# Optimization experiments

Hardware: AMD Instinct MI355X
Metric: run time of the kernel (lower is better)

Reference implementation:

```python
import jax, jax.numpy as jnp
import numpy as np

# dims
B, NB, T, NC = 16, 55, 512, 8          # batch, filter bands, time steps, CSP comps
D, L, H, E, K, F, C = 512, 6, 8, 8, 2, 2048, 2  # embed, depth, heads, experts, top_k, d_ff, classes
DH = D // H
IN = NB * NC  # 440
EPS = 1e-5


def _ln(x, s, b):
    m = x.mean(-1, keepdims=True)
    v = ((x - m) ** 2).mean(-1, keepdims=True)
    return (x - m) / jnp.sqrt(v + EPS) * s + b


def setup_inputs() -> dict:
    key = jax.random.key(0)
    ks = iter(jax.random.split(key, 64))
    n = lambda shape, s=0.02: jax.random.normal(next(ks), shape, jnp.float32) * s
    inp = {
        "x": jax.random.normal(next(ks), (B, NB, T, NC), jnp.float32),
        # frontend
        "proj_w": n((IN, D)), "proj_b": jnp.zeros((D,), jnp.float32),
        "pos": n((1, T, D)),
        "ln_pre_s": jnp.ones((D,), jnp.float32), "ln_pre_b": jnp.zeros((D,), jnp.float32),
        # stacked transformer-block params [L, ...]
        "ln1_s": jnp.ones((L, D), jnp.float32), "ln1_b": jnp.zeros((L, D), jnp.float32),
        "wq": n((L, D, D)), "bq": jnp.zeros((L, D), jnp.float32),
        "wk": n((L, D, D)), "bk": jnp.zeros((L, D), jnp.float32),
        "wv": n((L, D, D)), "bv": jnp.zeros((L, D), jnp.float32),
        "wo": n((L, D, D)), "bo": jnp.zeros((L, D), jnp.float32),
        "ln2_s": jnp.ones((L, D), jnp.float32), "ln2_b": jnp.zeros((L, D), jnp.float32),
        "gate_w": n((L, D, E)),
        "e_w1": n((L, E, D, F)), "e_b1": jnp.zeros((L, E, F), jnp.float32),
        "e_w2": n((L, E, F, D)), "e_b2": jnp.zeros((L, E, D), jnp.float32),
        # classifier head
        "ln_f_s": jnp.ones((D,), jnp.float32), "ln_f_b": jnp.zeros((D,), jnp.float32),
        "head_w": n((D, C)), "head_b": jnp.zeros((C,), jnp.float32),
    }
    return inp


def _moe(h, gw, w1, b1, w2, b2):
    # h: [N, D]; top-K softmax-gated mixture of GELU-FFN experts + load-balance aux loss
    N = h.shape[0]
    probs = jax.nn.softmax(h @ gw, axis=-1)                  # [N, E]
    vals, idx = jax.lax.top_k(probs, K)                      # [N, K]
    w = vals / vals.sum(-1, keepdims=True)                   # renormalized top-k weights
    disp = jax.nn.one_hot(idx, E, dtype=h.dtype)             # [N, K, E]
    combine = (disp * w[..., None]).sum(1)                   # [N, E]
    y = jnp.zeros_like(h)
    for e in range(E):  # small fixed expert loop
        y = y + combine[:, e:e + 1] * (jax.nn.gelu(h @ w1[e] + b1[e]) @ w2[e] + b2[e])
    frac = disp.mean((0, 1)) * K                             # fraction of tokens routed to each expert
    aux = E * jnp.sum(frac * probs.mean(0))
    return y, aux


def reference(x, proj_w, proj_b, pos, ln_pre_s, ln_pre_b, ln1_s, ln1_b, wq, bq, wk, bk,
              wv, bv, wo, bo, ln2_s, ln2_b, gate_w, e_w1, e_b1, e_w2, e_b2,
              ln_f_s, ln_f_b, head_w, head_b):
    b, nb, t, nc = x.shape
    h = x.transpose(0, 2, 1, 3).reshape(b, t, nb * nc) @ proj_w + proj_b  # [B,T,D]
    h = _ln(h + pos[:, :t, :], ln_pre_s, ln_pre_b)
    scale = DH ** -0.5
    total_aux = jnp.float32(0.0)
    for l in range(L):
        # pre-LN multi-head self-attention
        a = _ln(h, ln1_s[l], ln1_b[l])
        q = (a @ wq[l] + bq[l]).reshape(b, t, H, DH)
        k = (a @ wk[l] + bk[l]).reshape(b, t, H, DH)
        v = (a @ wv[l] + bv[l]).reshape(b, t, H, DH)
        att = jax.nn.softmax(jnp.einsum('bqhd,bkhd->bhqk', q, k) * scale, axis=-1)
        o = jnp.einsum('bhqk,bkhd->bqhd', att, v).reshape(b, t, D) @ wo[l] + bo[l]
        h = h + o
        # pre-LN MoE FFN
        m = _ln(h, ln2_s[l], ln2_b[l]).reshape(b * t, D)
        y, aux = _moe(m, gate_w[l], e_w1[l], e_b1[l], e_w2[l], e_b2[l])
        h = h + y.reshape(b, t, D)
        total_aux = total_aux + aux
    pooled = h.mean(axis=1)                                   # [B, D]
    logits = _ln(pooled, ln_f_s, ln_f_b) @ head_w + head_b    # [B, C]
    return logits, total_aux
```

## Files before the change

### kernel.cpp

```cpp
#include <hip/hip_runtime.h>
#include <stdint.h>

typedef unsigned short u16;
typedef unsigned int   u32;
typedef short bh8 __attribute__((ext_vector_type(8)));
typedef float f4  __attribute__((ext_vector_type(4)));

#define NTOK    8192
#define PADROWS 17408
#define MAXTILES 136

__device__ __forceinline__ u16 f2bf(float f){
  u32 u = __float_as_uint(f);
  return (u16)((u + 0x7fffu + ((u>>16)&1u)) >> 16);
}
__device__ __forceinline__ float bf2f(u16 h){ return __uint_as_float(((u32)h)<<16); }
__device__ __forceinline__ u32 pk2(float a, float b){ return (u32)f2bf(a) | ((u32)f2bf(b)<<16); }
__device__ __forceinline__ float gelu_f(float x){
  float u = 0.7978845608028654f*(x + 0.044715f*x*x*x);
  float t = 1.f - 2.f/(__expf(2.f*u)+1.f);
  return 0.5f*x*(1.f+t);
}
__device__ __forceinline__ void gload_lds16(const void* g, void* l){
  __builtin_amdgcn_global_load_lds((const __attribute__((address_space(1))) u32*)g,
                                   (__attribute__((address_space(3))) u32*)l, 16, 0, 0);
}

__global__ __launch_bounds__(256) void xpose_k(const float* __restrict__ x, u16* __restrict__ xt){
  int idx = blockIdx.x*256 + threadIdx.x;
  const float* src = x + (size_t)idx*8;
  float4 a = *(const float4*)src;
  float4 b = *(const float4*)(src+4);
  int t  = idx & 511;
  int nb = (idx>>9) % 55;
  int bb = (idx>>9) / 55;
  uint4 u;
  u.x = pk2(a.x,a.y); u.y = pk2(a.z,a.w); u.z = pk2(b.x,b.y); u.w = pk2(b.z,b.w);
  *(uint4*)&xt[((size_t)(bb*512+t))*448 + nb*8] = u;
}

__device__ __forceinline__ void tile_xpose(const float* __restrict__ src, u16* __restrict__ dst,
                                           int Ksrc, int N, int Kdst, float (*tile)[65])
{
  int tid = threadIdx.x;
  int k0 = blockIdx.y*64, n0 = blockIdx.x*64;
  #pragma unroll
  for (int p=0;p<4;++p){
    int r = p*16 + (tid>>4);
    int c4 = (tid&15)*4;
    int k = k0 + r;
    float4 v = (k < Ksrc) ? *(const float4*)&src[(size_t)k*N + n0 + c4] : (float4){0.f,0.f,0.f,0.f};
    tile[r][c4]=v.x; tile[r][c4+1]=v.y; tile[r][c4+2]=v.z; tile[r][c4+3]=v.w;
  }
  __syncthreads();
  #pragma unroll
  for (int p=0;p<2;++p){
    int rn = p*32 + (tid>>3);
    int ck = (tid&7)*8;
    uint4 u;
    u.x = pk2(tile[ck+0][rn], tile[ck+1][rn]);
    u.y = pk2(tile[ck+2][rn], tile[ck+3][rn]);
    u.z = pk2(tile[ck+4][rn], tile[ck+5][rn]);
    u.w = pk2(tile[ck+6][rn], tile[ck+7][rn]);
    *(uint4*)&dst[(size_t)(n0+rn)*Kdst + k0 + ck] = u;
  }
}

__global__ __launch_bounds__(256) void wconv_k(const float* __restrict__ src, u16* __restrict__ dst,
                                               int Ksrc, int N, int Kdst){
  __shared__ float tile[64][65];
  src += (size_t)blockIdx.z*Ksrc*N;
  dst += (size_t)blockIdx.z*N*Kdst;
  tile_xpose(src, dst, Ksrc, N, Kdst, tile);
}

__global__ __launch_bounds__(256) void wconv4_k(const float* __restrict__ wq, const float* __restrict__ wk,
    const float* __restrict__ wv, const float* __restrict__ wo,
    u16* __restrict__ qkvt, u16* __restrict__ wot)
{
  __shared__ float tile[64][65];
  int z = blockIdx.z;
  const float* src = (z==0)? wq : (z==1)? wk : (z==2)? wv : wo;
  u16* dst = (z==3) ? wot : qkvt + (size_t)z*512*512;
  tile_xpose(src, dst, 512, 512, 512, tile);
}

__global__ __launch_bounds__(256) void qkvb_k(const float* __restrict__ bq, const float* __restrict__ bk,
                                              const float* __restrict__ bv, float* __restrict__ qkvb){
  int idx = blockIdx.x*256 + threadIdx.x;
  int l = idx/1536, c = idx - l*1536;
  const float* s = (c<512)? bq : (c<1024)? bk : bv;
  qkvb[idx] = s[l*512 + (c&511)];
}

template<int MODE, bool GATHER>
__global__ __launch_bounds__(256) void gemm2_k(
    const u16* __restrict__ A, int lda,
    const u16* __restrict__ Bt, int ldb, int Ksteps,
    const float* __restrict__ biasBase,
    float* __restrict__ Cf, u16* __restrict__ Cb, int ldc,
    const int* __restrict__ tile_e, const int* __restrict__ toklist,
    const int* __restrict__ slotk, const float* __restrict__ wlist,
    float* __restrict__ y2, int expN)
{
  __shared__ __align__(16) u16 As[128*32];
  __shared__ __align__(16) u16 Bs[128*32];
  const int tid = threadIdx.x, lane = tid&63, w = tid>>6;
  const int wr = w>>1, wc = w&1;
  const int n0 = blockIdx.x*128, m0 = blockIdx.y*128;
  const u16* Bp = Bt;
  const float* bias = biasBase;
  if constexpr (MODE>=3){
    int e = tile_e[blockIdx.y];
    Bp   += (size_t)e*(size_t)expN*(size_t)ldb;
    bias += (size_t)e*(size_t)expN;
  }
  const u16* asrc0; const u16* asrc1; const u16* bsrc0; const u16* bsrc1;
  {
    int idx0 = tid, row0 = idx0>>2, sp0 = idx0&3, ks0 = sp0 ^ ((row0>>1)&3);
    int idx1 = 256+tid, row1 = idx1>>2, sp1 = idx1&3, ks1 = sp1 ^ ((row1>>1)&3);
    size_t ar0 = GATHER ? (size_t)toklist[m0+row0] : (size_t)(m0+row0);
    size_t ar1 = GATHER ? (size_t)toklist[m0+row1] : (size_t)(m0+row1);
    asrc0 = A + ar0*(size_t)lda + ks0*8;
    asrc1 = A + ar1*(size_t)lda + ks1*8;
    bsrc0 = Bp + (size_t)(n0+row0)*ldb + ks0*8;
    bsrc1 = Bp + (size_t)(n0+row1)*ldb + ks1*8;
  }
  f4 acc[4][4];
  #pragma unroll
  for (int i=0;i<4;++i)
    #pragma unroll
    for (int j=0;j<4;++j) acc[i][j] = (f4){0.f,0.f,0.f,0.f};

  for (int kt=0; kt<Ksteps; ++kt){
    gload_lds16(asrc0, &As[tid*8]);
    gload_lds16(asrc1, &As[(256+tid)*8]);
    gload_lds16(bsrc0, &Bs[tid*8]);
    gload_lds16(bsrc1, &Bs[(256+tid)*8]);
    asrc0 += 32; asrc1 += 32; bsrc0 += 32; bsrc1 += 32;
    __syncthreads();
    bh8 af[4], bf[4];
    const int q = lane>>4;
    #pragma unroll
    for (int mf=0;mf<4;++mf){
      int r = wr*64 + mf*16 + (lane&15);
      af[mf] = *(const bh8*)&As[r*32 + (q ^ ((r>>1)&3))*8];
    }
    #pragma unroll
    for (int nf=0;nf<4;++nf){
      int r = wc*64 + nf*16 + (lane&15);
      bf[nf] = *(const bh8*)&Bs[r*32 + (q ^ ((r>>1)&3))*8];
    }
    #pragma unroll
    for (int mf=0;mf<4;++mf)
      #pragma unroll
      for (int nf=0;nf<4;++nf)
        acc[mf][nf] = __builtin_amdgcn_mfma_f32_16x16x32_bf16(af[mf], bf[nf], acc[mf][nf], 0, 0, 0);
    __syncthreads();
  }
  #pragma unroll
  for (int mf=0;mf<4;++mf){
    #pragma unroll
    for (int nf=0;nf<4;++nf){
      f4 d = acc[mf][nf];
      int ncol = n0 + wc*64 + nf*16 + (lane&15);
      float bv = bias[ncol];
      #pragma unroll
      for (int r=0;r<4;++r){
        int mrow = m0 + wr*64 + mf*16 + (lane>>4)*4 + r;
        float val = d[r] + bv;
        if constexpr (MODE==0){
          Cf[(size_t)mrow*ldc + ncol] = val;
        } else if constexpr (MODE==1){
          Cb[(size_t)mrow*ldc + ncol] = f2bf(val);
        } else if constexpr (MODE==2){
          Cf[(size_t)mrow*ldc + ncol] += val;
        } else if constexpr (MODE==3){
          Cb[(size_t)mrow*ldc + ncol] = f2bf(gelu_f(val));
        } else {
          int sk = slotk[mrow];
          if (sk >= 0){
            int tok = toklist[mrow];
            y2[((size_t)sk*NTOK + (size_t)tok)*512 + ncol] = wlist[mrow]*val;
          }
        }
      }
    }
  }
}

template<bool ADDPOS, bool OUTF32>
__global__ __launch_bounds__(256) void ln_k(const float* __restrict__ X, const float* __restrict__ pos,
    const float* __restrict__ sc, const float* __restrict__ bi,
    float* __restrict__ outF, u16* __restrict__ outB)
{
  int tid=threadIdx.x, lane=tid&63, w=tid>>6;
  int row = blockIdx.x*4 + w;
  const float* xr = X + (size_t)row*512 + lane*8;
  float x[8];
  float4 v0 = *(const float4*)xr;
  float4 v1 = *(const float4*)(xr+4);
  x[0]=v0.x;x[1]=v0.y;x[2]=v0.z;x[3]=v0.w;x[4]=v1.x;x[5]=v1.y;x[6]=v1.z;x[7]=v1.w;
  if constexpr (ADDPOS){
    const float* pr = pos + (size_t)(row&511)*512 + lane*8;
    float4 p0 = *(const float4*)pr, p1 = *(const float4*)(pr+4);
    x[0]+=p0.x;x[1]+=p0.y;x[2]+=p0.z;x[3]+=p0.w;x[4]+=p1.x;x[5]+=p1.y;x[6]+=p1.z;x[7]+=p1.w;
  }
  float sm=0.f, sq=0.f;
  #pragma unroll
  for (int i=0;i<8;++i){ sm+=x[i]; sq+=x[i]*x[i]; }
  #pragma unroll
  for (int mk=1; mk<64; mk<<=1){ sm += __shfl_xor(sm, mk); sq += __shfl_xor(sq, mk); }
  float mean = sm*(1.f/512.f);
  float var  = sq*(1.f/512.f) - mean*mean;
  float rstd = rsqrtf(var + 1e-5f);
  int d0 = lane*8;
  float4 s0 = *(const float4*)(sc+d0), s1 = *(const float4*)(sc+d0+4);
  float4 b0 = *(const float4*)(bi+d0), b1 = *(const float4*)(bi+d0+4);
  float y[8];
  y[0]=(x[0]-mean)*rstd*s0.x+b0.x; y[1]=(x[1]-mean)*rstd*s0.y+b0.y;
  y[2]=(x[2]-mean)*rstd*s0.z+b0.z; y[3]=(x[3]-mean)*rstd*s0.w+b0.w;
  y[4]=(x[4]-mean)*rstd*s1.x+b1.x; y[5]=(x[5]-mean)*rstd*s1.y+b1.y;
  y[6]=(x[6]-mean)*rstd*s1.z+b1.z; y[7]=(x[7]-mean)*rstd*s1.w+b1.w;
  if constexpr (OUTF32){
    float4 o0 = {y[0],y[1],y[2],y[3]}, o1 = {y[4],y[5],y[6],y[7]};
    *(float4*)(outF + (size_t)row*512 + d0)     = o0;
    *(float4*)(outF + (size_t)row*512 + d0 + 4) = o1;
  } else {
    uint4 u; u.x=pk2(y[0],y[1]); u.y=pk2(y[2],y[3]); u.z=pk2(y[4],y[5]); u.w=pk2(y[6],y[7]);
    *(uint4*)&outB[(size_t)row*512 + d0] = u;
  }
}

__global__ __launch_bounds__(256) void attn_k(const u16* __restrict__ QKV, u16* __restrict__ Og)
{
  __shared__ __align__(16) u16 VT[64*72];
  __shared__ __align__(16) u16 PS[4][16*80];
  int tid=threadIdx.x, lane=tid&63, w=tid>>6;
  int qt=blockIdx.x, hh=blockIdx.y, bb=blockIdx.z;
  size_t base  = (size_t)bb*512*1536 + (size_t)hh*64;
  size_t obase = (size_t)bb*512*512  + (size_t)hh*64;
  int qrow0 = qt*64 + w*16;
  bh8 qf[2];
  #pragma unroll
  for (int kf=0;kf<2;++kf)
    qf[kf] = *(const bh8*)&QKV[ base + (size_t)(qrow0 + (lane&15))*1536 + kf*32 + (lane>>4)*8 ];
  f4 oacc[4];
  #pragma unroll
  for (int i=0;i<4;++i) oacc[i] = (f4){0.f,0.f,0.f,0.f};
  float mrun[4] = {-1e30f,-1e30f,-1e30f,-1e30f};
  float lrun[4] = {0.f,0.f,0.f,0.f};
  const float scale = 0.125f;

  for (int kt=0; kt<8; ++kt){
    __syncthreads();
    #pragma unroll
    for (int r2=0;r2<2;++r2){
      int idx = r2*256 + tid;
      int dh0 = (idx&7)*8, key = idx>>3;
      const u16* src = &QKV[ base + (size_t)(kt*64+key)*1536 + 1024 + dh0 ];
      uint4 raw = *(const uint4*)src;
      u32 rw[4] = {raw.x, raw.y, raw.z, raw.w};
      #pragma unroll
      for (int j=0;j<4;++j){
        VT[(dh0+2*j  )*72 + key] = (u16)(rw[j]&0xffff);
        VT[(dh0+2*j+1)*72 + key] = (u16)(rw[j]>>16);
      }
    }
    f4 s[4];
    #pragma unroll
    for (int nf=0;nf<4;++nf){
      size_t krow = base + (size_t)(kt*64+nf*16+(lane&15))*1536 + 512 + (lane>>4)*8;
      bh8 k0 = *(const bh8*)&QKV[krow];
      bh8 k1 = *(const bh8*)&QKV[krow+32];
      f4 z = (f4){0.f,0.f,0.f,0.f};
      z = __builtin_amdgcn_mfma_f32_16x16x32_bf16(qf[0], k0, z, 0,0,0);
      z = __builtin_amdgcn_mfma_f32_16x16x32_bf16(qf[1], k1, z, 0,0,0);
      s[nf] = z;
    }
    float pe[4][4];
    #pragma unroll
    for (int r=0;r<4;++r){
      float sv0=s[0][r]*scale, sv1=s[1][r]*scale, sv2=s[2][r]*scale, sv3=s[3][r]*scale;
      float mt = fmaxf(fmaxf(sv0,sv1), fmaxf(sv2,sv3));
      #pragma unroll
      for (int mk=1; mk<16; mk<<=1) mt = fmaxf(mt, __shfl_xor(mt, mk));
      float mn = fmaxf(mrun[r], mt);
      float sf = __expf(mrun[r]-mn);
      float p0=__expf(sv0-mn), p1=__expf(sv1-mn), p2=__expf(sv2-mn), p3=__expf(sv3-mn);
      pe[0][r]=p0; pe[1][r]=p1; pe[2][r]=p2; pe[3][r]=p3;
      float rs = p0+p1+p2+p3;
      #pragma unroll
      for (int mk=1; mk<16; mk<<=1) rs += __shfl_xor(rs, mk);
      lrun[r] = lrun[r]*sf + rs;
      mrun[r] = mn;
      #pragma unroll
      for (int df=0;df<4;++df) oacc[df][r] *= sf;
    }
    #pragma unroll
    for (int nf=0;nf<4;++nf)
      #pragma unroll
      for (int r=0;r<4;++r)
        PS[w][ ((lane>>4)*4+r)*80 + nf*16 + (lane&15) ] = f2bf(pe[nf][r]);
    __syncthreads();
    #pragma unroll
    for (int ks=0;ks<2;++ks){
      bh8 pa = *(const bh8*)&PS[w][ (lane&15)*80 + ks*32 + (lane>>4)*8 ];
      #pragma unroll
      for (int df=0;df<4;++df){
        bh8 vb = *(const bh8*)&VT[ (df*16+(lane&15))*72 + ks*32 + (lane>>4)*8 ];
        oacc[df] = __builtin_amdgcn_mfma_f32_16x16x32_bf16(pa, vb, oacc[df], 0,0,0);
      }
    }
  }
  #pragma unroll
  for (int df=0;df<4;++df)
    #pragma unroll
    for (int r=0;r<4;++r){
      int qr = qrow0 + (lane>>4)*4 + r;
      float ov = oacc[df][r] / lrun[r];
      Og[ obase + (size_t)qr*512 + df*16 + (lane&15) ] = f2bf(ov);
    }
}

__global__ __launch_bounds__(256) void route_k(const u16* __restrict__ m, const float* __restrict__ gw,
    float* __restrict__ psum, int* __restrict__ cnt, int* __restrict__ t2e, float* __restrict__ t2w)
{
  __shared__ float ps[8]; __shared__ int cs[8];
  int tid=threadIdx.x, lane=tid&63, w=tid>>6;
  if (tid<8){ ps[tid]=0.f; cs[tid]=0; }
  __syncthreads();
  for (int it=0; it<4; ++it){
    int t = blockIdx.x*16 + w*4 + it;
    const u16* row = m + (size_t)t*512 + lane*8;
    uint4 raw = *(const uint4*)row;
    u32 rw[4] = {raw.x,raw.y,raw.z,raw.w};
    float x[8];
    #pragma unroll
    for (int j=0;j<4;++j){ x[2*j]=bf2f((u16)(rw[j]&0xffff)); x[2*j+1]=bf2f((u16)(rw[j]>>16)); }
    float acc[8] = {0,0,0,0,0,0,0,0};
    #pragma unroll
    for (int j=0;j<8;++j){
      const float* g = gw + (size_t)(lane*8+j)*8;
      float4 g0 = *(const float4*)g, g1 = *(const float4*)(g+4);
      acc[0]+=x[j]*g0.x; acc[1]+=x[j]*g0.y; acc[2]+=x[j]*g0.z; acc[3]+=x[j]*g0.w;
      acc[4]+=x[j]*g1.x; acc[5]+=x[j]*g1.y; acc[6]+=x[j]*g1.z; acc[7]+=x[j]*g1.w;
    }
    #pragma unroll
    for (int mk=1; mk<64; mk<<=1)
      #pragma unroll
      for (int e=0;e<8;++e) acc[e] += __shfl_xor(acc[e], mk);
    if (lane==0){
      float mx=acc[0];
      #pragma unroll
      for (int e=1;e<8;++e) mx = fmaxf(mx, acc[e]);
      float pe[8], tot=0.f;
      #pragma unroll
      for (int e=0;e<8;++e){ pe[e]=__expf(acc[e]-mx); tot+=pe[e]; }
      float inv = 1.f/tot;
      #pragma unroll
      for (int e=0;e<8;++e) pe[e]*=inv;
      int e0=0; float v0=pe[0];
      #pragma unroll
      for (int e=1;e<8;++e) if (pe[e]>v0){ v0=pe[e]; e0=e; }
      int e1=-1; float v1=-1.f;
      #pragma unroll
      for (int e=0;e<8;++e) if (e!=e0 && pe[e]>v1){ v1=pe[e]; e1=e; }
      float invw = 1.f/(v0+v1);
      t2e[2*t]=e0; t2w[2*t]=v0*invw; t2e[2*t+1]=e1; t2w[2*t+1]=v1*invw;
      #pragma unroll
      for (int e=0;e<8;++e) atomicAdd(&ps[e], pe[e]);
      atomicAdd(&cs[e0],1); atomicAdd(&cs[e1],1);
    }
  }
  __syncthreads();
  if (tid<8){ atomicAdd(&psum[tid], ps[tid]); atomicAdd(&cnt[tid], cs[tid]); }
}

__global__ __launch_bounds__(256) void offsets_k(const int* __restrict__ cnt, const float* __restrict__ psum,
    int* __restrict__ offs, int* __restrict__ fill, int* __restrict__ tile_e,
    int* __restrict__ toklist, int* __restrict__ slotk, float* __restrict__ wlist, float* __restrict__ auxp)
{
  int tid = threadIdx.x;
  if (tid==0){
    int off=0; float auxl=0.f;
    for (int e=0;e<8;++e){
      offs[e] = off;
      int reg = (cnt[e]+127)&~127;
      int t0 = off>>7, t1 = (off+reg)>>7;
      for (int t=t0;t<t1;++t) tile_e[t]=e;
      off += reg;
      auxl += ((float)cnt[e]*(1.f/8192.f)) * (psum[e]*(1.f/8192.f));
    }
    for (int t=off>>7; t<MAXTILES; ++t) tile_e[t]=0;
    auxp[0] += 8.f*auxl;
  }
  if (tid<8) fill[tid]=0;
  for (int i=tid;i<PADROWS;i+=256){ toklist[i]=0; slotk[i]=-1; wlist[i]=0.f; }
}

__global__ __launch_bounds__(256) void scatter_k(const int* __restrict__ t2e, const float* __restrict__ t2w,
    const int* __restrict__ offs, int* __restrict__ fill,
    int* __restrict__ toklist, int* __restrict__ slotk, float* __restrict__ wlist)
{
  int t = blockIdx.x*256 + threadIdx.x;
  #pragma unroll
  for (int kk=0;kk<2;++kk){
    int e = t2e[2*t+kk];
    int p = atomicAdd(&fill[e], 1);
    int i = offs[e] + p;
    toklist[i] = t; slotk[i] = kk; wlist[i] = t2w[2*t+kk];
  }
}

__global__ __launch_bounds__(256) void add_k(float* __restrict__ h, const float* __restrict__ y2){
  const int total = NTOK*512/4;
  for (int idx = blockIdx.x*256+threadIdx.x; idx < total; idx += gridDim.x*256){
    float4 a = ((const float4*)y2)[idx];
    float4 b = ((const float4*)y2)[total + idx];
    float4 hv = ((const float4*)h)[idx];
    hv.x += a.x+b.x; hv.y += a.y+b.y; hv.z += a.z+b.z; hv.w += a.w+b.w;
    ((float4*)h)[idx] = hv;
  }
}

__global__ __launch_bounds__(256) void pool_k(const float* __restrict__ h, float* __restrict__ pooled){
  int idx = blockIdx.x*256 + threadIdx.x;
  int bb = idx>>9, d = idx&511;
  const float* p = h + (size_t)bb*512*512 + d;
  float s=0.f;
  for (int t=0;t<512;++t) s += p[(size_t)t*512];
  pooled[idx] = s*(1.f/512.f);
}

__global__ __launch_bounds__(256) void head_k(const float* __restrict__ pooled,
    const float* __restrict__ sc, const float* __restrict__ bi,
    const float* __restrict__ hw, const float* __restrict__ hb,
    const float* __restrict__ auxp, float* __restrict__ out)
{
  int tid=threadIdx.x, lane=tid&63, w=tid>>6;
  for (int i=0;i<4;++i){
    int row = w*4+i;
    const float* xr = pooled + (size_t)row*512 + lane*8;
    float x[8];
    float4 v0 = *(const float4*)xr, v1 = *(const float4*)(xr+4);
    x[0]=v0.x;x[1]=v0.y;x[2]=v0.z;x[3]=v0.w;x[4]=v1.x;x[5]=v1.y;x[6]=v1.z;x[7]=v1.w;
    float sm=0.f, sq=0.f;
    #pragma unroll
    for (int j=0;j<8;++j){ sm+=x[j]; sq+=x[j]*x[j]; }
    #pragma unroll
    for (int mk=1; mk<64; mk<<=1){ sm += __shfl_xor(sm, mk); sq += __shfl_xor(sq, mk); }
    float mean = sm*(1.f/512.f);
    float rstd = rsqrtf(sq*(1.f/512.f) - mean*mean + 1e-5f);
    int d0 = lane*8;
    float c0=0.f, c1=0.f;
    #pragma unroll
    for (int j=0;j<8;++j){
      float yv = (x[j]-mean)*rstd*sc[d0+j] + bi[d0+j];
      c0 += yv*hw[(d0+j)*2]; c1 += yv*hw[(d0+j)*2+1];
    }
    #pragma unroll
    for (int mk=1; mk<64; mk<<=1){ c0 += __shfl_xor(c0, mk); c1 += __shfl_xor(c1, mk); }
    if (lane==0){ out[row*2+0] = c0 + hb[0]; out[row*2+1] = c1 + hb[1]; }
  }
  if (tid==0) out[32] = auxp[0];
}

extern "C" void kernel_launch(void* const* d_in, const int* in_sizes, int n_in,
                              void* d_out, int out_size, void* d_ws, size_t ws_size,
                              hipStream_t stream)
{
  (void)in_sizes; (void)n_in; (void)out_size; (void)ws_size;
  const float* x      = (const float*)d_in[0];
  const float* proj_w = (const float*)d_in[1];
  const float* proj_b = (const float*)d_in[2];
  const float* pos    = (const float*)d_in[3];
  const float* ln_pre_s=(const float*)d_in[4];
  const float* ln_pre_b=(const float*)d_in[5];
  const float* ln1_s  = (const float*)d_in[6];
  const float* ln1_b  = (const float*)d_in[7];
  const float* wq     = (const float*)d_in[8];
  const float* bq     = (const float*)d_in[9];
  const float* wk     = (const float*)d_in[10];
  const float* bk     = (const float*)d_in[11];
  const float* wv     = (const float*)d_in[12];
  const float* bv     = (const float*)d_in[13];
  const float* wo     = (const float*)d_in[14];
  const float* bo     = (const float*)d_in[15];
  const float* ln2_s  = (const float*)d_in[16];
  const float* ln2_b  = (const float*)d_in[17];
  const float* gate_w = (const float*)d_in[18];
  const float* e_w1   = (const float*)d_in[19];
  const float* e_b1   = (const float*)d_in[20];
  const float* e_w2   = (const float*)d_in[21];
  const float* e_b2   = (const float*)d_in[22];
  const float* ln_f_s = (const float*)d_in[23];
  const float* ln_f_b = (const float*)d_in[24];
  const float* head_w = (const float*)d_in[25];
  const float* head_b = (const float*)d_in[26];

  char* base = (char*)d_ws;
  size_t off = 0;
  auto carve = [&](size_t bytes)->char*{
    char* r = base + off; off += (bytes + 255) & ~(size_t)255; return r;
  };
  u16*   xt      = (u16*)  carve((size_t)8192*448*2);
  float* h       = (float*)carve((size_t)8192*512*4);
  u16*   a       = (u16*)  carve((size_t)8192*512*2);
  u16*   qkv     = (u16*)  carve((size_t)8192*1536*2);
  u16*   ob      = (u16*)  carve((size_t)8192*512*2);
  u16*   hidden  = (u16*)  carve((size_t)PADROWS*2048*2);
  float* y2      = (float*)carve((size_t)2*NTOK*512*4);
  u16*   projt   = (u16*)  carve((size_t)512*448*2);
  u16*   qkvt    = (u16*)  carve((size_t)1536*512*2);
  u16*   wot     = (u16*)  carve((size_t)512*512*2);
  u16*   w1t     = (u16*)  carve((size_t)8*2048*512*2);
  u16*   w2t     = (u16*)  carve((size_t)8*512*2048*2);
  float* qkvb    = (float*)carve((size_t)6*1536*4);
  int*   toklist = (int*)  carve(PADROWS*4);
  int*   slotk   = (int*)  carve(PADROWS*4);
  float* wlist   = (float*)carve(PADROWS*4);
  int*   tile_e  = (int*)  carve(256*4);
  int*   rcnt    = (int*)  carve(96);
  float* psum    = (float*)(rcnt+8);
  int*   fill    = rcnt+16;
  int*   offs    = (int*)  carve(64);
  int*   t2e     = (int*)  carve(16384*4);
  float* t2w     = (float*)carve(16384*4);
  float* pooled  = (float*)carve(8192*4);
  float* auxp    = (float*)carve(256);

  hipMemsetAsync(xt, 0, (size_t)8192*448*2, stream);
  hipMemsetAsync(auxp, 0, 4, stream);

  xpose_k<<<1760, 256, 0, stream>>>(x, xt);
  wconv_k<<<dim3(8,7,1), 256, 0, stream>>>(proj_w, projt, 440, 512, 448);
  qkvb_k<<<36, 256, 0, stream>>>(bq, bk, bv, qkvb);
  gemm2_k<0,false><<<dim3(4,64), 256, 0, stream>>>(xt, 448, projt, 448, 14, proj_b,
      h, nullptr, 512, nullptr, nullptr, nullptr, nullptr, nullptr, 0);
  ln_k<true,true><<<2048, 256, 0, stream>>>(h, pos, ln_pre_s, ln_pre_b, h, nullptr);

  for (int l=0; l<6; ++l){
    wconv4_k<<<dim3(8,8,4), 256, 0, stream>>>(wq+(size_t)l*512*512, wk+(size_t)l*512*512,
        wv+(size_t)l*512*512, wo+(size_t)l*512*512, qkvt, wot);
    ln_k<false,false><<<2048, 256, 0, stream>>>(h, nullptr, ln1_s+(size_t)l*512, ln1_b+(size_t)l*512, nullptr, a);
    gemm2_k<1,false><<<dim3(12,64), 256, 0, stream>>>(a, 512, qkvt, 512, 16, qkvb+(size_t)l*1536,
        nullptr, qkv, 1536, nullptr, nullptr, nullptr, nullptr, nullptr, 0);
    attn_k<<<dim3(8,8,16), 256, 0, stream>>>(qkv, ob);
    gemm2_k<2,false><<<dim3(4,64), 256, 0, stream>>>(ob, 512, wot, 512, 16, bo+(size_t)l*512,
        h, nullptr, 512, nullptr, nullptr, nullptr, nullptr, nullptr, 0);
    ln_k<false,false><<<2048, 256, 0, stream>>>(h, nullptr, ln2_s+(size_t)l*512, ln2_b+(size_t)l*512, nullptr, a);
    hipMemsetAsync(rcnt, 0, 64, stream);
    route_k<<<512, 256, 0, stream>>>(a, gate_w+(size_t)l*512*8, psum, rcnt, t2e, t2w);
    offsets_k<<<1, 256, 0, stream>>>(rcnt, psum, offs, fill, tile_e, toklist, slotk, wlist, auxp);
    scatter_k<<<32, 256, 0, stream>>>(t2e, t2w, offs, fill, toklist, slotk, wlist);
    wconv_k<<<dim3(32,8,8), 256, 0, stream>>>(e_w1+(size_t)l*8*512*2048, w1t, 512, 2048, 512);
    wconv_k<<<dim3(8,32,8), 256, 0, stream>>>(e_w2+(size_t)l*8*2048*512, w2t, 2048, 512, 2048);
    gemm2_k<3,true ><<<dim3(16,MAXTILES), 256, 0, stream>>>(a, 512, w1t, 512, 16,
        e_b1 + (size_t)l*8*2048, nullptr, hidden, 2048, tile_e, toklist, slotk, wlist, nullptr, 2048);
    gemm2_k<4,false><<<dim3(4,MAXTILES), 256, 0, stream>>>(hidden, 2048, w2t, 2048, 64,
        e_b2 + (size_t)l*8*512, nullptr, nullptr, 512, tile_e, toklist, slotk, wlist, y2, 512);
    add_k<<<1024, 256, 0, stream>>>(h, y2);
  }

  pool_k<<<32, 256, 0, stream>>>(h, pooled);
  head_k<<<1, 256, 0, stream>>>(pooled, ln_f_s, ln_f_b, head_w, head_b, auxp, (float*)d_out);
}
```

Baseline: 2.469 ms.

## Use head-major QKV layout, double-buffer swizzled VT, atomically combine MoE outputs into h

The QKV projection now writes a head-sliced layout [slab][token][64], so attention reads Q, K and V contiguously per head. Attention double-buffers the transposed V tile, drops one barrier per key tile, and XOR-swizzles the V and P LDS indices to cut bank conflicts. The second MoE GEMM atomically adds weighted expert outputs straight into h, which removes the y2 buffer and the add_k pass. The float atomics make summation order nondeterministic and add contention on h, and the lone remaining barrier per iteration must still keep the double-buffered V tile safe.

```diff
diff --git a/kernel.cpp b/kernel.cpp
--- a/kernel.cpp
+++ b/kernel.cpp
@@ -101,7 +101,7 @@
     float* __restrict__ Cf, u16* __restrict__ Cb, int ldc,
     const int* __restrict__ tile_e, const int* __restrict__ toklist,
     const int* __restrict__ slotk, const float* __restrict__ wlist,
-    float* __restrict__ y2, int expN)
+    int expN)
 {
   __shared__ __align__(16) u16 As[128*32];
   __shared__ __align__(16) u16 Bs[128*32];
@@ -172,7 +172,8 @@
         if constexpr (MODE==0){
           Cf[(size_t)mrow*ldc + ncol] = val;
         } else if constexpr (MODE==1){
-          Cb[(size_t)mrow*ldc + ncol] = f2bf(val);
+          int slab = ncol>>6, dh = ncol&63;
+          Cb[((size_t)slab*NTOK + (size_t)mrow)*64 + dh] = f2bf(val);
         } else if constexpr (MODE==2){
           Cf[(size_t)mrow*ldc + ncol] += val;
         } else if constexpr (MODE==3){
@@ -181,7 +182,7 @@
           int sk = slotk[mrow];
           if (sk >= 0){
             int tok = toklist[mrow];
-            y2[((size_t)sk*NTOK + (size_t)tok)*512 + ncol] = wlist[mrow]*val;
+            atomicAdd(&Cf[(size_t)tok*512 + ncol], wlist[mrow]*val);
           }
         }
       }
@@ -234,17 +235,19 @@
 
 __global__ __launch_bounds__(256) void attn_k(const u16* __restrict__ QKV, u16* __restrict__ Og)
 {
-  __shared__ __align__(16) u16 VT[64*72];
-  __shared__ __align__(16) u16 PS[4][16*80];
+  __shared__ __align__(16) u16 VT[2][64*72];
+  __shared__ __align__(16) u16 PS[4][16*72];
   int tid=threadIdx.x, lane=tid&63, w=tid>>6;
   int qt=blockIdx.x, hh=blockIdx.y, bb=blockIdx.z;
-  size_t base  = (size_t)bb*512*1536 + (size_t)hh*64;
-  size_t obase = (size_t)bb*512*512  + (size_t)hh*64;
+  const u16* Qh = QKV + ((size_t)hh     *NTOK + (size_t)bb*512)*64;
+  const u16* Kh = QKV + ((size_t)(8+hh) *NTOK + (size_t)bb*512)*64;
+  const u16* Vh = QKV + ((size_t)(16+hh)*NTOK + (size_t)bb*512)*64;
+  size_t obase = (size_t)bb*512*512 + (size_t)hh*64;
   int qrow0 = qt*64 + w*16;
   bh8 qf[2];
   #pragma unroll
   for (int kf=0;kf<2;++kf)
-    qf[kf] = *(const bh8*)&QKV[ base + (size_t)(qrow0 + (lane&15))*1536 + kf*32 + (lane>>4)*8 ];
+    qf[kf] = *(const bh8*)&Qh[ (size_t)(qrow0 + (lane&15))*64 + kf*32 + (lane>>4)*8 ];
   f4 oacc[4];
   #pragma unroll
   for (int i=0;i<4;++i) oacc[i] = (f4){0.f,0.f,0.f,0.f};
@@ -253,26 +256,27 @@
   const float scale = 0.125f;
 
   for (int kt=0; kt<8; ++kt){
-    __syncthreads();
+    const int buf = kt&1;
     #pragma unroll
     for (int r2=0;r2<2;++r2){
       int idx = r2*256 + tid;
-      int dh0 = (idx&7)*8, key = idx>>3;
-      const u16* src = &QKV[ base + (size_t)(kt*64+key)*1536 + 1024 + dh0 ];
-      uint4 raw = *(const uint4*)src;
+      int dhg = idx&7;
+      int dh0 = dhg*8, key = idx>>3;
+      uint4 raw = *(const uint4*)&Vh[ (size_t)(kt*64+key)*64 + dh0 ];
+      int kx = key ^ (dhg<<3);
       u32 rw[4] = {raw.x, raw.y, raw.z, raw.w};
       #pragma unroll
       for (int j=0;j<4;++j){
-        VT[(dh0+2*j  )*72 + key] = (u16)(rw[j]&0xffff);
-        VT[(dh0+2*j+1)*72 + key] = (u16)(rw[j]>>16);
+        VT[buf][(dh0+2*j  )*72 + kx] = (u16)(rw[j]&0xffff);
+        VT[buf][(dh0+2*j+1)*72 + kx] = (u16)(rw[j]>>16);
       }
     }
     f4 s[4];
     #pragma unroll
     for (int nf=0;nf<4;++nf){
-      size_t krow = base + (size_t)(kt*64+nf*16+(lane&15))*1536 + 512 + (lane>>4)*8;
-      bh8 k0 = *(const bh8*)&QKV[krow];
-      bh8 k1 = *(const bh8*)&QKV[krow+32];
+      size_t krow = (size_t)(kt*64+nf*16+(lane&15))*64 + (lane>>4)*8;
+      bh8 k0 = *(const bh8*)&Kh[krow];
+      bh8 k1 = *(const bh8*)&Kh[krow+32];
       f4 z = (f4){0.f,0.f,0.f,0.f};
       z = __builtin_amdgcn_mfma_f32_16x16x32_bf16(qf[0], k0, z, 0,0,0);
       z = __builtin_amdgcn_mfma_f32_16x16x32_bf16(qf[1], k1, z, 0,0,0);
@@ -301,14 +305,16 @@
     for (int nf=0;nf<4;++nf)
       #pragma unroll
       for (int r=0;r<4;++r)
-        PS[w][ ((lane>>4)*4+r)*80 + nf*16 + (lane&15) ] = f2bf(pe[nf][r]);
+        PS[w][ ((lane>>4)*4+r)*72 + nf*16 + (lane&15) ] = f2bf(pe[nf][r]);
     __syncthreads();
     #pragma unroll
     for (int ks=0;ks<2;++ks){
-      bh8 pa = *(const bh8*)&PS[w][ (lane&15)*80 + ks*32 + (lane>>4)*8 ];
+      bh8 pa = *(const bh8*)&PS[w][ (lane&15)*72 + ks*32 + (lane>>4)*8 ];
       #pragma unroll
       for (int df=0;df<4;++df){
-        bh8 vb = *(const bh8*)&VT[ (df*16+(lane&15))*72 + ks*32 + (lane>>4)*8 ];
+        int dh = df*16 + (lane&15);
+        int sgrp = (dh>>3)&7;
+        bh8 vb = *(const bh8*)&VT[buf][ dh*72 + ((ks*4 + (lane>>4)) ^ sgrp)*8 ];
         oacc[df] = __builtin_amdgcn_mfma_f32_16x16x32_bf16(pa, vb, oacc[df], 0,0,0);
       }
     }
@@ -410,17 +416,6 @@
     int p = atomicAdd(&fill[e], 1);
     int i = offs[e] + p;
     toklist[i] = t; slotk[i] = kk; wlist[i] = t2w[2*t+kk];
-  }
-}
-
-__global__ __launch_bounds__(256) void add_k(float* __restrict__ h, const float* __restrict__ y2){
-  const int total = NTOK*512/4;
-  for (int idx = blockIdx.x*256+threadIdx.x; idx < total; idx += gridDim.x*256){
-    float4 a = ((const float4*)y2)[idx];
-    float4 b = ((const float4*)y2)[total + idx];
-    float4 hv = ((const float4*)h)[idx];
-    hv.x += a.x+b.x; hv.y += a.y+b.y; hv.z += a.z+b.z; hv.w += a.w+b.w;
-    ((float4*)h)[idx] = hv;
   }
 }
 
@@ -510,7 +505,6 @@
   u16*   qkv     = (u16*)  carve((size_t)8192*1536*2);
   u16*   ob      = (u16*)  carve((size_t)8192*512*2);
   u16*   hidden  = (u16*)  carve((size_t)PADROWS*2048*2);
-  float* y2      = (float*)carve((size_t)2*NTOK*512*4);
   u16*   projt   = (u16*)  carve((size_t)512*448*2);
   u16*   qkvt    = (u16*)  carve((size_t)1536*512*2);
   u16*   wot     = (u16*)  carve((size_t)512*512*2);
@@ -537,7 +531,7 @@
   wconv_k<<<dim3(8,7,1), 256, 0, stream>>>(proj_w, projt, 440, 512, 448);
   qkvb_k<<<36, 256, 0, stream>>>(bq, bk, bv, qkvb);
   gemm2_k<0,false><<<dim3(4,64), 256, 0, stream>>>(xt, 448, projt, 448, 14, proj_b,
-      h, nullptr, 512, nullptr, nullptr, nullptr, nullptr, nullptr, 0);
+      h, nullptr, 512, nullptr, nullptr, nullptr, nullptr, 0);
   ln_k<true,true><<<2048, 256, 0, stream>>>(h, pos, ln_pre_s, ln_pre_b, h, nullptr);
 
   for (int l=0; l<6; ++l){
@@ -545,10 +539,10 @@
         wv+(size_t)l*512*512, wo+(size_t)l*512*512, qkvt, wot);
     ln_k<false,false><<<2048, 256, 0, stream>>>(h, nullptr, ln1_s+(size_t)l*512, ln1_b+(size_t)l*512, nullptr, a);
     gemm2_k<1,false><<<dim3(12,64), 256, 0, stream>>>(a, 512, qkvt, 512, 16, qkvb+(size_t)l*1536,
-        nullptr, qkv, 1536, nullptr, nullptr, nullptr, nullptr, nullptr, 0);
+        nullptr, qkv, 1536, nullptr, nullptr, nullptr, nullptr, 0);
     attn_k<<<dim3(8,8,16), 256, 0, stream>>>(qkv, ob);
     gemm2_k<2,false><<<dim3(4,64), 256, 0, stream>>>(ob, 512, wot, 512, 16, bo+(size_t)l*512,
-        h, nullptr, 512, nullptr, nullptr, nullptr, nullptr, nullptr, 0);
+        h, nullptr, 512, nullptr, nullptr, nullptr, nullptr, 0);
     ln_k<false,false><<<2048, 256, 0, stream>>>(h, nullptr, ln2_s+(size_t)l*512, ln2_b+(size_t)l*512, nullptr, a);
     hipMemsetAsync(rcnt, 0, 64, stream);
     route_k<<<512, 256, 0, stream>>>(a, gate_w+(size_t)l*512*8, psum, rcnt, t2e, t2w);
@@ -557,10 +551,9 @@
     wconv_k<<<dim3(32,8,8), 256, 0, stream>>>(e_w1+(size_t)l*8*512*2048, w1t, 512, 2048, 512);
     wconv_k<<<dim3(8,32,8), 256, 0, stream>>>(e_w2+(size_t)l*8*2048*512, w2t, 2048, 512, 2048);
     gemm2_k<3,true ><<<dim3(16,MAXTILES), 256, 0, stream>>>(a, 512, w1t, 512, 16,
-        e_b1 + (size_t)l*8*2048, nullptr, hidden, 2048, tile_e, toklist, slotk, wlist, nullptr, 2048);
+        e_b1 + (size_t)l*8*2048, nullptr, hidden, 2048, tile_e, toklist, slotk, wlist, 2048);
     gemm2_k<4,false><<<dim3(4,MAXTILES), 256, 0, stream>>>(hidden, 2048, w2t, 2048, 64,
-        e_b2 + (size_t)l*8*512, nullptr, nullptr, 512, tile_e, toklist, slotk, wlist, y2, 512);
-    add_k<<<1024, 256, 0, stream>>>(h, y2);
+        e_b2 + (size_t)l*8*512, h, nullptr, 512, tile_e, toklist, slotk, wlist, 512);
   }
 
   pool_k<<<32, 256, 0, stream>>>(h, pooled);
```

Result: no change. 2.475 ms (+0.3%).
